# Performance work log

Measured on AMD Instinct MI355X. Metric: run time of the kernel, lower is better.

Reference implementation:

```python
import jax, jax.numpy as jnp
import numpy as np
from jax import lax

NUM_LAYERS = 3
NUM_QUBITS = 8
BATCH = 131072
DIM = 2 ** NUM_QUBITS  # 256


def _rot_mats(params):
    # params: (L, Q, 3) angles for RX, RY, RZ. Returns combined U = RZ @ RY @ RX, (L, Q, 2, 2) complex64.
    half = params * 0.5
    cx = jnp.cos(half[..., 0]).astype(jnp.complex64)
    sx = jnp.sin(half[..., 0]).astype(jnp.complex64)
    cy = jnp.cos(half[..., 1]).astype(jnp.complex64)
    sy = jnp.sin(half[..., 1]).astype(jnp.complex64)
    ezm = jnp.exp(-1j * half[..., 2]).astype(jnp.complex64)
    ezp = jnp.exp(1j * half[..., 2]).astype(jnp.complex64)
    zero = jnp.zeros_like(cx)
    RX = jnp.stack([jnp.stack([cx, -1j * sx], -1), jnp.stack([-1j * sx, cx], -1)], -2)
    RY = jnp.stack([jnp.stack([cy, -sy], -1), jnp.stack([sy, cy], -1)], -2)
    RZ = jnp.stack([jnp.stack([ezm, zero], -1), jnp.stack([zero, ezp], -1)], -2)
    return jnp.einsum('lqij,lqjk,lqkm->lqim', RZ, RY, RX)


def _apply_1q(state, U, wire):
    # state: (B, 2,2,...,2); wire w lives on axis w+1 (PennyLane wire 0 = most significant bit)
    ax = wire + 1
    return jnp.moveaxis(jnp.tensordot(U, state, axes=((1,), (ax,))), 0, ax)


def _apply_cnot(state, ctrl, tgt):
    c_ax, t_ax = ctrl + 1, tgt + 1
    s0 = lax.index_in_dim(state, 0, axis=c_ax, keepdims=True)
    s1 = lax.index_in_dim(state, 1, axis=c_ax, keepdims=True)
    s1 = jnp.flip(s1, axis=t_ax)
    return jnp.concatenate([s0, s1], axis=c_ax)


def _circuit(params, state_re, state_im):
    U = _rot_mats(params)  # (L, Q, 2, 2)
    state = (state_re + 1j * state_im).astype(jnp.complex64)
    state = state.reshape((state.shape[0],) + (2,) * NUM_QUBITS)
    for l in range(NUM_LAYERS):
        for q in range(NUM_QUBITS):
            state = _apply_1q(state, U[l, q], q)
        for q in range(NUM_QUBITS):
            state = _apply_cnot(state, q, (q + 1) % NUM_QUBITS)
    state = state.reshape(state.shape[0], DIM)
    # probability that wire 0 measures |0>: sum |amp|^2 over first half of amplitudes
    half = state[:, : DIM // 2]
    return jnp.sum(half.real ** 2 + half.imag ** 2, axis=1).astype(jnp.float32)


def setup_inputs() -> dict:
    key = jax.random.key(0)
    k1, k2, k3 = jax.random.split(key, 3)
    params = jax.random.uniform(k1, (NUM_LAYERS, NUM_QUBITS, 3), dtype=jnp.float32)
    sr = jax.random.normal(k2, (BATCH, DIM), dtype=jnp.float32)
    si = jax.random.normal(k3, (BATCH, DIM), dtype=jnp.float32)
    norm = jnp.sqrt(jnp.sum(sr ** 2 + si ** 2, axis=1, keepdims=True))
    return {"params": params, "state_re": sr / norm, "state_im": si / norm}


def reference(params, state_re, state_im):
    return _circuit(params, state_re, state_im)
```

## Files before the change

kernel.cpp:

```cpp
#include <hip/hip_runtime.h>
#include <stdint.h>

#define NLAYERS 3
#define NQ 8
#define DIM 256
#define HALF 128
#define BATCH 131072

typedef float  f32x4  __attribute__((ext_vector_type(4)));
typedef __bf16 bf16x8 __attribute__((ext_vector_type(8)));

__device__ __forceinline__ unsigned short f2bf(float f){
    union { float f; uint32_t u; } v; v.f = f;
    uint32_t u = v.u;
    u += 0x7fffu + ((u >> 16) & 1u);
    return (unsigned short)(u >> 16);
}

__device__ __forceinline__ float2 cmul(float2 a, float2 b){
    return make_float2(a.x*b.x - a.y*b.y, a.x*b.y + a.y*b.x);
}

__device__ __forceinline__ void gload_lds16(void* lds, const void* g){
    __builtin_amdgcn_global_load_lds(
        (const __attribute__((address_space(1))) unsigned int*)g,
        (__attribute__((address_space(3))) unsigned int*)lds,
        16, 0, 0);
}

__global__ __launch_bounds__(256) void build_w_kernel(const float* __restrict__ params,
                                                      unsigned short* __restrict__ W){
    __shared__ float2 st[2][DIM];
    __shared__ float2 gm[NLAYERS*NQ][4];
    const int j = blockIdx.x;
    const int i = threadIdx.x;

    if (i < NLAYERS*NQ){
        const float* pp = params + i*3;
        float hx = 0.5f*pp[0], hy = 0.5f*pp[1], hz = 0.5f*pp[2];
        float cx = cosf(hx), sx = sinf(hx);
        float cy = cosf(hy), sy = sinf(hy);
        float cz = cosf(hz), sz = sinf(hz);
        float2 ezm = make_float2(cz, -sz), ezp = make_float2(cz, sz);
        float2 m00 = make_float2( cy*cx,  sy*sx);
        float2 m01 = make_float2(-sy*cx, -cy*sx);
        float2 m10 = make_float2( sy*cx, -cy*sx);
        float2 m11 = make_float2( cy*cx, -sy*sx);
        gm[i][0] = cmul(ezm, m00);
        gm[i][1] = cmul(ezm, m01);
        gm[i][2] = cmul(ezp, m10);
        gm[i][3] = cmul(ezp, m11);
    }

    int psrc = i;
    #pragma unroll
    for (int q = NQ-1; q >= 0; --q){
        int c  = 7 - q;
        int tb = 7 - ((q + 1) & 7);
        psrc = ((psrc >> c) & 1) ? (psrc ^ (1 << tb)) : psrc;
    }

    int cur = 0;
    st[0][i] = make_float2(i == j ? 1.0f : 0.0f, 0.0f);
    __syncthreads();

    for (int l = 0; l < NLAYERS; ++l){
        for (int q = 0; q < NQ; ++q){
            float2 U0a = gm[l*NQ+q][0], U0b = gm[l*NQ+q][1];
            float2 U1a = gm[l*NQ+q][2], U1b = gm[l*NQ+q][3];
            int p  = 7 - q;
            int bs = (i >> p) & 1;
            int i0 = i & ~(1 << p), i1 = i | (1 << p);
            float2 a0 = st[cur][i0], a1 = st[cur][i1];
            float2 ua = bs ? U1a : U0a;
            float2 ub = bs ? U1b : U0b;
            float2 r;
            r.x = ua.x*a0.x - ua.y*a0.y + ub.x*a1.x - ub.y*a1.y;
            r.y = ua.x*a0.y + ua.y*a0.x + ub.x*a1.y + ub.y*a1.x;
            st[cur ^ 1][i] = r;
            cur ^= 1;
            __syncthreads();
        }
        float2 r = st[cur][psrc];
        st[cur ^ 1][i] = r;
        cur ^= 1;
        __syncthreads();
    }

    const int m = i & 127;
    float2 a = st[cur][m];
    const uint32_t off = (uint32_t)m*256u
                       + ((((uint32_t)j >> 3) ^ ((uint32_t)m & 7u)) << 3)
                       + ((uint32_t)j & 7u);
    if (i < 128) W[off]          = f2bf(a.x);
    else         W[32768u + off] = f2bf(a.y);
}

__global__ __launch_bounds__(1024) void qform2_kernel(const float* __restrict__ sr,
                                                      const float* __restrict__ si,
                                                      const unsigned short* __restrict__ W,
                                                      float* __restrict__ out){
    __shared__ unsigned short Bs[65536];

    const int tid  = threadIdx.x;
    const int lane = tid & 63;
    const int w    = tid >> 6;
    const int l15  = lane & 15;
    const int quad = lane >> 4;

    #pragma unroll
    for (int r = 0; r < 8; ++r){
        const int c = w*8 + r;
        gload_lds16(&Bs[c*512], W + (size_t)c*512 + lane*8);
    }
    __syncthreads();

    const size_t row0 = (size_t)blockIdx.x * 512 + (size_t)w * 32;

    #pragma unroll 1
    for (int t = 0; t < 2; ++t){
        const float* ar = sr + (row0 + (size_t)(t*16 + l15)) * DIM;
        const float* ai = si + (row0 + (size_t)(t*16 + l15)) * DIM;

        f32x4 accR[8], accI[8];
        const f32x4 z = {0.0f, 0.0f, 0.0f, 0.0f};
        #pragma unroll
        for (int jf = 0; jf < 8; ++jf){ accR[jf] = z; accI[jf] = z; }

        float4 r0 = *(const float4*)(ar + quad*8);
        float4 r1 = *(const float4*)(ar + quad*8 + 4);
        float4 q0 = *(const float4*)(ai + quad*8);
        float4 q1 = *(const float4*)(ai + quad*8 + 4);

        #pragma unroll 1
        for (int ks = 0; ks < 8; ++ks){
            union { float4 v; uint32_t u[4]; } ha, hb;
            union { uint32_t u[4]; bf16x8 f; } pr, pi, pn;
            ha.v = r0; hb.v = r1;
            pr.u[0] = __builtin_amdgcn_perm(ha.u[1], ha.u[0], 0x07060302);
            pr.u[1] = __builtin_amdgcn_perm(ha.u[3], ha.u[2], 0x07060302);
            pr.u[2] = __builtin_amdgcn_perm(hb.u[1], hb.u[0], 0x07060302);
            pr.u[3] = __builtin_amdgcn_perm(hb.u[3], hb.u[2], 0x07060302);
            ha.v = q0; hb.v = q1;
            pi.u[0] = __builtin_amdgcn_perm(ha.u[1], ha.u[0], 0x07060302);
            pi.u[1] = __builtin_amdgcn_perm(ha.u[3], ha.u[2], 0x07060302);
            pi.u[2] = __builtin_amdgcn_perm(hb.u[1], hb.u[0], 0x07060302);
            pi.u[3] = __builtin_amdgcn_perm(hb.u[3], hb.u[2], 0x07060302);
            pn.u[0] = pi.u[0] ^ 0x80008000u;
            pn.u[1] = pi.u[1] ^ 0x80008000u;
            pn.u[2] = pi.u[2] ^ 0x80008000u;
            pn.u[3] = pi.u[3] ^ 0x80008000u;
            const bf16x8 fr = pr.f;
            const bf16x8 fi = pi.f;
            const bf16x8 fn = pn.f;

            const int nk = (ks < 7) ? (ks + 1) : 7;
            r0 = *(const float4*)(ar + nk*32 + quad*8);
            r1 = *(const float4*)(ar + nk*32 + quad*8 + 4);
            q0 = *(const float4*)(ai + nk*32 + quad*8);
            q1 = *(const float4*)(ai + nk*32 + quad*8 + 4);

            const int ub = l15*256 + (((ks*4 + quad) ^ (l15 & 7)) << 3);

            #pragma unroll
            for (int jf = 0; jf < 8; ++jf){
                const bf16x8 br = *(const bf16x8*)&Bs[ub + jf*4096];
                const bf16x8 bi = *(const bf16x8*)&Bs[32768 + ub + jf*4096];
                accR[jf] = __builtin_amdgcn_mfma_f32_16x16x32_bf16(fr, br, accR[jf], 0, 0, 0);
                accR[jf] = __builtin_amdgcn_mfma_f32_16x16x32_bf16(fn, bi, accR[jf], 0, 0, 0);
                accI[jf] = __builtin_amdgcn_mfma_f32_16x16x32_bf16(fr, bi, accI[jf], 0, 0, 0);
                accI[jf] = __builtin_amdgcn_mfma_f32_16x16x32_bf16(fi, br, accI[jf], 0, 0, 0);
            }
        }

        float s[4];
        #pragma unroll
        for (int r = 0; r < 4; ++r){
            float tt = 0.0f;
            #pragma unroll
            for (int jf = 0; jf < 8; ++jf){
                const float vr = accR[jf][r];
                const float vi = accI[jf][r];
                tt += vr*vr + vi*vi;
            }
            tt += __shfl_xor(tt, 1);
            tt += __shfl_xor(tt, 2);
            tt += __shfl_xor(tt, 4);
            tt += __shfl_xor(tt, 8);
            s[r] = tt;
        }
        if (l15 == 0){
            float4 o; o.x = s[0]; o.y = s[1]; o.z = s[2]; o.w = s[3];
            *(float4*)(out + row0 + t*16 + quad*4) = o;
        }
    }
}

extern "C" void kernel_launch(void* const* d_in, const int* in_sizes, int n_in,
                              void* d_out, int out_size, void* d_ws, size_t ws_size,
                              hipStream_t stream){
    const float* params = (const float*)d_in[0];
    const float* sr     = (const float*)d_in[1];
    const float* si     = (const float*)d_in[2];
    unsigned short* Wimg = (unsigned short*)d_ws;
    float* out          = (float*)d_out;

    build_w_kernel<<<dim3(DIM), dim3(256), 0, stream>>>(params, Wimg);
    qform2_kernel<<<dim3(256), dim3(1024), 0, stream>>>(sr, si, Wimg, out);
}
```

Measured before the change: 297.5 us.

## Deepen global prefetch to four stages across fully unrolled K loop

Merges the two row-tile iterations into one fully unrolled loop of 16 K-steps. It keeps four stages of register prefetch in flight, so global loads for step k+4 are issued while step k computes, and loads for the second tile start before the first tile's reduction. It also raises wave priority around the MFMA block with s_setprio. The cost is higher register pressure from 16 extra float4 buffers plus the full unroll, which may reduce occupancy or cause spills.

```diff
diff --git a/kernel.cpp b/kernel.cpp
--- a/kernel.cpp
+++ b/kernel.cpp
@@ -107,6 +107,7 @@
     const int w    = tid >> 6;
     const int l15  = lane & 15;
     const int quad = lane >> 4;
+    const int xq   = l15 & 7;
 
     #pragma unroll
     for (int r = 0; r < 8; ++r){
@@ -116,82 +117,101 @@
     __syncthreads();
 
     const size_t row0 = (size_t)blockIdx.x * 512 + (size_t)w * 32;
-
-    #pragma unroll 1
-    for (int t = 0; t < 2; ++t){
-        const float* ar = sr + (row0 + (size_t)(t*16 + l15)) * DIM;
-        const float* ai = si + (row0 + (size_t)(t*16 + l15)) * DIM;
-
-        f32x4 accR[8], accI[8];
-        const f32x4 z = {0.0f, 0.0f, 0.0f, 0.0f};
+    const float* ar0 = sr + (row0 + l15) * DIM;
+    const float* ai0 = si + (row0 + l15) * DIM;
+    const float* ar1 = ar0 + (size_t)16 * DIM;
+    const float* ai1 = ai0 + (size_t)16 * DIM;
+
+    f32x4 accR[8], accI[8];
+    const f32x4 z = {0.0f, 0.0f, 0.0f, 0.0f};
+    #pragma unroll
+    for (int jf = 0; jf < 8; ++jf){ accR[jf] = z; accI[jf] = z; }
+
+    float4 R0[4], R1[4], Q0[4], Q1[4];
+
+    #pragma unroll
+    for (int p = 0; p < 4; ++p){
+        R0[p] = *(const float4*)(ar0 + p*32 + quad*8);
+        R1[p] = *(const float4*)(ar0 + p*32 + quad*8 + 4);
+        Q0[p] = *(const float4*)(ai0 + p*32 + quad*8);
+        Q1[p] = *(const float4*)(ai0 + p*32 + quad*8 + 4);
+    }
+
+    #pragma unroll
+    for (int kab = 0; kab < 16; ++kab){
+        const int ks = kab & 7;
+        const int s  = kab & 3;
+
+        union { float4 v; uint32_t u[4]; } ha, hb;
+        union { uint32_t u[4]; bf16x8 f; } pr, pi, pn;
+        ha.v = R0[s]; hb.v = R1[s];
+        pr.u[0] = __builtin_amdgcn_perm(ha.u[1], ha.u[0], 0x07060302);
+        pr.u[1] = __builtin_amdgcn_perm(ha.u[3], ha.u[2], 0x07060302);
+        pr.u[2] = __builtin_amdgcn_perm(hb.u[1], hb.u[0], 0x07060302);
+        pr.u[3] = __builtin_amdgcn_perm(hb.u[3], hb.u[2], 0x07060302);
+        ha.v = Q0[s]; hb.v = Q1[s];
+        pi.u[0] = __builtin_amdgcn_perm(ha.u[1], ha.u[0], 0x07060302);
+        pi.u[1] = __builtin_amdgcn_perm(ha.u[3], ha.u[2], 0x07060302);
+        pi.u[2] = __builtin_amdgcn_perm(hb.u[1], hb.u[0], 0x07060302);
+        pi.u[3] = __builtin_amdgcn_perm(hb.u[3], hb.u[2], 0x07060302);
+        pn.u[0] = pi.u[0] ^ 0x80008000u;
+        pn.u[1] = pi.u[1] ^ 0x80008000u;
+        pn.u[2] = pi.u[2] ^ 0x80008000u;
+        pn.u[3] = pi.u[3] ^ 0x80008000u;
+        const bf16x8 fr = pr.f;
+        const bf16x8 fi = pi.f;
+        const bf16x8 fn = pn.f;
+
+        if (kab + 4 < 16){
+            const int nk = kab + 4;
+            const float* pra = (nk < 8) ? ar0 : ar1;
+            const float* pia = (nk < 8) ? ai0 : ai1;
+            const int kk = nk & 7;
+            R0[s] = *(const float4*)(pra + kk*32 + quad*8);
+            R1[s] = *(const float4*)(pra + kk*32 + quad*8 + 4);
+            Q0[s] = *(const float4*)(pia + kk*32 + quad*8);
+            Q1[s] = *(const float4*)(pia + kk*32 + quad*8 + 4);
+        }
+
+        const int ub = l15*256 + ((((ks<<2) + quad) ^ xq) << 3);
+        __builtin_amdgcn_s_setprio(1);
         #pragma unroll
-        for (int jf = 0; jf < 8; ++jf){ accR[jf] = z; accI[jf] = z; }
-
-        float4 r0 = *(const float4*)(ar + quad*8);
-        float4 r1 = *(const float4*)(ar + quad*8 + 4);
-        float4 q0 = *(const float4*)(ai + quad*8);
-        float4 q1 = *(const float4*)(ai + quad*8 + 4);
-
-        #pragma unroll 1
-        for (int ks = 0; ks < 8; ++ks){
-            union { float4 v; uint32_t u[4]; } ha, hb;
-            union { uint32_t u[4]; bf16x8 f; } pr, pi, pn;
-            ha.v = r0; hb.v = r1;
-            pr.u[0] = __builtin_amdgcn_perm(ha.u[1], ha.u[0], 0x07060302);
-            pr.u[1] = __builtin_amdgcn_perm(ha.u[3], ha.u[2], 0x07060302);
-            pr.u[2] = __builtin_amdgcn_perm(hb.u[1], hb.u[0], 0x07060302);
-            pr.u[3] = __builtin_amdgcn_perm(hb.u[3], hb.u[2], 0x07060302);
-            ha.v = q0; hb.v = q1;
-            pi.u[0] = __builtin_amdgcn_perm(ha.u[1], ha.u[0], 0x07060302);
-            pi.u[1] = __builtin_amdgcn_perm(ha.u[3], ha.u[2], 0x07060302);
-            pi.u[2] = __builtin_amdgcn_perm(hb.u[1], hb.u[0], 0x07060302);
-            pi.u[3] = __builtin_amdgcn_perm(hb.u[3], hb.u[2], 0x07060302);
-            pn.u[0] = pi.u[0] ^ 0x80008000u;
-            pn.u[1] = pi.u[1] ^ 0x80008000u;
-            pn.u[2] = pi.u[2] ^ 0x80008000u;
-            pn.u[3] = pi.u[3] ^ 0x80008000u;
-            const bf16x8 fr = pr.f;
-            const bf16x8 fi = pi.f;
-            const bf16x8 fn = pn.f;
-
-            const int nk = (ks < 7) ? (ks + 1) : 7;
-            r0 = *(const float4*)(ar + nk*32 + quad*8);
-            r1 = *(const float4*)(ar + nk*32 + quad*8 + 4);
-            q0 = *(const float4*)(ai + nk*32 + quad*8);
-            q1 = *(const float4*)(ai + nk*32 + quad*8 + 4);
-
-            const int ub = l15*256 + (((ks*4 + quad) ^ (l15 & 7)) << 3);
-
+        for (int jf = 0; jf < 8; ++jf){
+            const bf16x8 br = *(const bf16x8*)&Bs[ub + jf*4096];
+            const bf16x8 bi = *(const bf16x8*)&Bs[32768 + ub + jf*4096];
+            accR[jf] = __builtin_amdgcn_mfma_f32_16x16x32_bf16(fr, br, accR[jf], 0, 0, 0);
+            accR[jf] = __builtin_amdgcn_mfma_f32_16x16x32_bf16(fn, bi, accR[jf], 0, 0, 0);
+            accI[jf] = __builtin_amdgcn_mfma_f32_16x16x32_bf16(fr, bi, accI[jf], 0, 0, 0);
+            accI[jf] = __builtin_amdgcn_mfma_f32_16x16x32_bf16(fi, br, accI[jf], 0, 0, 0);
+        }
+        __builtin_amdgcn_s_setprio(0);
+
+        if (ks == 7){
+            const int t = kab >> 3;
+            float sacc[4];
             #pragma unroll
-            for (int jf = 0; jf < 8; ++jf){
-                const bf16x8 br = *(const bf16x8*)&Bs[ub + jf*4096];
-                const bf16x8 bi = *(const bf16x8*)&Bs[32768 + ub + jf*4096];
-                accR[jf] = __builtin_amdgcn_mfma_f32_16x16x32_bf16(fr, br, accR[jf], 0, 0, 0);
-                accR[jf] = __builtin_amdgcn_mfma_f32_16x16x32_bf16(fn, bi, accR[jf], 0, 0, 0);
-                accI[jf] = __builtin_amdgcn_mfma_f32_16x16x32_bf16(fr, bi, accI[jf], 0, 0, 0);
-                accI[jf] = __builtin_amdgcn_mfma_f32_16x16x32_bf16(fi, br, accI[jf], 0, 0, 0);
+            for (int r = 0; r < 4; ++r){
+                float tt = 0.0f;
+                #pragma unroll
+                for (int jf = 0; jf < 8; ++jf){
+                    const float vr = accR[jf][r];
+                    const float vi = accI[jf][r];
+                    tt += vr*vr + vi*vi;
+                }
+                tt += __shfl_xor(tt, 1);
+                tt += __shfl_xor(tt, 2);
+                tt += __shfl_xor(tt, 4);
+                tt += __shfl_xor(tt, 8);
+                sacc[r] = tt;
             }
-        }
-
-        float s[4];
-        #pragma unroll
-        for (int r = 0; r < 4; ++r){
-            float tt = 0.0f;
-            #pragma unroll
-            for (int jf = 0; jf < 8; ++jf){
-                const float vr = accR[jf][r];
-                const float vi = accI[jf][r];
-                tt += vr*vr + vi*vi;
+            if (l15 == 0){
+                float4 o; o.x = sacc[0]; o.y = sacc[1]; o.z = sacc[2]; o.w = sacc[3];
+                *(float4*)(out + row0 + t*16 + quad*4) = o;
             }
-            tt += __shfl_xor(tt, 1);
-            tt += __shfl_xor(tt, 2);
-            tt += __shfl_xor(tt, 4);
-            tt += __shfl_xor(tt, 8);
-            s[r] = tt;
-        }
-        if (l15 == 0){
-            float4 o; o.x = s[0]; o.y = s[1]; o.z = s[2]; o.w = s[3];
-            *(float4*)(out + row0 + t*16 + quad*4) = o;
+            if (t == 0){
+                #pragma unroll
+                for (int jf = 0; jf < 8; ++jf){ accR[jf] = z; accI[jf] = z; }
+            }
         }
     }
 }
```

New measurement: 336.3 us. 13.1% more time.

## Deepen row prefetch to a full 16-row tile with 512-thread blocks

Applied to the files above, without the earlier changes.

Each block drops to 512 threads (8 waves), and each wave now handles 64 rows in four 16-row tiles instead of 32 rows in two. The loads for the next tile, all eight K-slices of it, are issued in register slots as each slice is consumed, so a whole tile is in flight instead of one slice ahead. MFMA sections get raised wave priority through s_setprio. The aim is to hide HBM latency on the streaming input reads, at the cost of much higher register pressure and fewer waves per CU to hide latency with.

```diff
diff --git a/kernel.cpp b/kernel.cpp
--- a/kernel.cpp
+++ b/kernel.cpp
@@ -96,10 +96,56 @@
     else         W[32768u + off] = f2bf(a.y);
 }
 
-__global__ __launch_bounds__(1024) void qform2_kernel(const float* __restrict__ sr,
-                                                      const float* __restrict__ si,
-                                                      const unsigned short* __restrict__ W,
-                                                      float* __restrict__ out){
+
+#define LOADSLOT(S, PR, PI)                          \
+    sR0_##S = *(const float4*)((PR) + (S)*32);       \
+    sR1_##S = *(const float4*)((PR) + (S)*32 + 4);   \
+    sQ0_##S = *(const float4*)((PI) + (S)*32);       \
+    sQ1_##S = *(const float4*)((PI) + (S)*32 + 4);
+
+#define STEP(S)                                                                 \
+{                                                                               \
+    union { float4 v; uint32_t u[4]; } ha_, hb_;                                \
+    union { uint32_t u[4]; bf16x8 f; } pr_, pi_, pn_;                           \
+    ha_.v = sR0_##S; hb_.v = sR1_##S;                                           \
+    pr_.u[0] = __builtin_amdgcn_perm(ha_.u[1], ha_.u[0], 0x07060302);           \
+    pr_.u[1] = __builtin_amdgcn_perm(ha_.u[3], ha_.u[2], 0x07060302);           \
+    pr_.u[2] = __builtin_amdgcn_perm(hb_.u[1], hb_.u[0], 0x07060302);           \
+    pr_.u[3] = __builtin_amdgcn_perm(hb_.u[3], hb_.u[2], 0x07060302);           \
+    ha_.v = sQ0_##S; hb_.v = sQ1_##S;                                           \
+    pi_.u[0] = __builtin_amdgcn_perm(ha_.u[1], ha_.u[0], 0x07060302);           \
+    pi_.u[1] = __builtin_amdgcn_perm(ha_.u[3], ha_.u[2], 0x07060302);           \
+    pi_.u[2] = __builtin_amdgcn_perm(hb_.u[1], hb_.u[0], 0x07060302);           \
+    pi_.u[3] = __builtin_amdgcn_perm(hb_.u[3], hb_.u[2], 0x07060302);           \
+    pn_.u[0] = pi_.u[0] ^ 0x80008000u;                                          \
+    pn_.u[1] = pi_.u[1] ^ 0x80008000u;                                          \
+    pn_.u[2] = pi_.u[2] ^ 0x80008000u;                                          \
+    pn_.u[3] = pi_.u[3] ^ 0x80008000u;                                          \
+    const bf16x8 fr_ = pr_.f;                                     \
+    const bf16x8 fi_ = pi_.f;                                     \
+    const bf16x8 fn_ = pn_.f;                                    \
+      \
+    LOADSLOT(S, narq, naiq)                                                     \
+    const int ub_ = l15*256 + ((((S<<2) + quad) ^ xq) << 3);                    \
+    const unsigned short* bre_ = &Bs[ub_];                                      \
+    const unsigned short* bim_ = &Bs[32768 + ub_];                              \
+    __builtin_amdgcn_s_setprio(1);                                              \
+    _Pragma("unroll")                                                           \
+    for (int jf = 0; jf < 8; ++jf){                                             \
+        const bf16x8 br = *(const bf16x8*)(bre_ + jf*4096);                     \
+        const bf16x8 bi = *(const bf16x8*)(bim_ + jf*4096);                     \
+        accR[jf] = __builtin_amdgcn_mfma_f32_16x16x32_bf16(fr_, br, accR[jf], 0, 0, 0); \
+        accR[jf] = __builtin_amdgcn_mfma_f32_16x16x32_bf16(fn_, bi, accR[jf], 0, 0, 0); \
+        accI[jf] = __builtin_amdgcn_mfma_f32_16x16x32_bf16(fr_, bi, accI[jf], 0, 0, 0); \
+        accI[jf] = __builtin_amdgcn_mfma_f32_16x16x32_bf16(fi_, br, accI[jf], 0, 0, 0); \
+    }                                                                           \
+    __builtin_amdgcn_s_setprio(0);                                              \
+}
+
+__global__ __launch_bounds__(512, 2) void qform2_kernel(const float* __restrict__ sr,
+                                                        const float* __restrict__ si,
+                                                        const unsigned short* __restrict__ W,
+                                                        float* __restrict__ out){
     __shared__ unsigned short Bs[65536];
 
     const int tid  = threadIdx.x;
@@ -107,92 +153,86 @@
     const int w    = tid >> 6;
     const int l15  = lane & 15;
     const int quad = lane >> 4;
+    const int xq   = l15 & 7;
+
+    const size_t rowbase = (size_t)blockIdx.x * 512 + (size_t)w * 64;
+
+    const float* arq = sr + (rowbase + l15) * DIM + quad*8;
+    const float* aiq = si + (rowbase + l15) * DIM + quad*8;
+
+    float4 sR0_0, sR1_0, sQ0_0, sQ1_0;
+    float4 sR0_1, sR1_1, sQ0_1, sQ1_1;
+    float4 sR0_2, sR1_2, sQ0_2, sQ1_2;
+    float4 sR0_3, sR1_3, sQ0_3, sQ1_3;
+    float4 sR0_4, sR1_4, sQ0_4, sQ1_4;
+    float4 sR0_5, sR1_5, sQ0_5, sQ1_5;
+    float4 sR0_6, sR1_6, sQ0_6, sQ1_6;
+    float4 sR0_7, sR1_7, sQ0_7, sQ1_7;
+
+    LOADSLOT(0, arq, aiq)
+    LOADSLOT(1, arq, aiq)
+    LOADSLOT(2, arq, aiq)
+    LOADSLOT(3, arq, aiq)
+    LOADSLOT(4, arq, aiq)
+    LOADSLOT(5, arq, aiq)
+    LOADSLOT(6, arq, aiq)
+    LOADSLOT(7, arq, aiq)
 
     #pragma unroll
-    for (int r = 0; r < 8; ++r){
-        const int c = w*8 + r;
+    for (int r = 0; r < 16; ++r){
+        const int c = w*16 + r;
         gload_lds16(&Bs[c*512], W + (size_t)c*512 + lane*8);
     }
     __syncthreads();
 
-    const size_t row0 = (size_t)blockIdx.x * 512 + (size_t)w * 32;
+    f32x4 accR[8], accI[8];
+    const f32x4 z = {0.0f, 0.0f, 0.0f, 0.0f};
+    #pragma unroll
+    for (int jf = 0; jf < 8; ++jf){ accR[jf] = z; accI[jf] = z; }
 
     #pragma unroll 1
-    for (int t = 0; t < 2; ++t){
-        const float* ar = sr + (row0 + (size_t)(t*16 + l15)) * DIM;
-        const float* ai = si + (row0 + (size_t)(t*16 + l15)) * DIM;
-
-        f32x4 accR[8], accI[8];
-        const f32x4 z = {0.0f, 0.0f, 0.0f, 0.0f};
-        #pragma unroll
-        for (int jf = 0; jf < 8; ++jf){ accR[jf] = z; accI[jf] = z; }
-
-        float4 r0 = *(const float4*)(ar + quad*8);
-        float4 r1 = *(const float4*)(ar + quad*8 + 4);
-        float4 q0 = *(const float4*)(ai + quad*8);
-        float4 q1 = *(const float4*)(ai + quad*8 + 4);
-
-        #pragma unroll 1
-        for (int ks = 0; ks < 8; ++ks){
-            union { float4 v; uint32_t u[4]; } ha, hb;
-            union { uint32_t u[4]; bf16x8 f; } pr, pi, pn;
-            ha.v = r0; hb.v = r1;
-            pr.u[0] = __builtin_amdgcn_perm(ha.u[1], ha.u[0], 0x07060302);
-            pr.u[1] = __builtin_amdgcn_perm(ha.u[3], ha.u[2], 0x07060302);
-            pr.u[2] = __builtin_amdgcn_perm(hb.u[1], hb.u[0], 0x07060302);
-            pr.u[3] = __builtin_amdgcn_perm(hb.u[3], hb.u[2], 0x07060302);
-            ha.v = q0; hb.v = q1;
-            pi.u[0] = __builtin_amdgcn_perm(ha.u[1], ha.u[0], 0x07060302);
-            pi.u[1] = __builtin_amdgcn_perm(ha.u[3], ha.u[2], 0x07060302);
-            pi.u[2] = __builtin_amdgcn_perm(hb.u[1], hb.u[0], 0x07060302);
-            pi.u[3] = __builtin_amdgcn_perm(hb.u[3], hb.u[2], 0x07060302);
-            pn.u[0] = pi.u[0] ^ 0x80008000u;
-            pn.u[1] = pi.u[1] ^ 0x80008000u;
-            pn.u[2] = pi.u[2] ^ 0x80008000u;
-            pn.u[3] = pi.u[3] ^ 0x80008000u;
-            const bf16x8 fr = pr.f;
-            const bf16x8 fi = pi.f;
-            const bf16x8 fn = pn.f;
-
-            const int nk = (ks < 7) ? (ks + 1) : 7;
-            r0 = *(const float4*)(ar + nk*32 + quad*8);
-            r1 = *(const float4*)(ar + nk*32 + quad*8 + 4);
-            q0 = *(const float4*)(ai + nk*32 + quad*8);
-            q1 = *(const float4*)(ai + nk*32 + quad*8 + 4);
-
-            const int ub = l15*256 + (((ks*4 + quad) ^ (l15 & 7)) << 3);
-
+    for (int t = 0; t < 4; ++t){
+        const float* narq = (t < 3) ? (arq + 16*DIM) : arq;
+        const float* naiq = (t < 3) ? (aiq + 16*DIM) : aiq;
+
+        STEP(0)
+        STEP(1)
+        STEP(2)
+        STEP(3)
+        STEP(4)
+        STEP(5)
+        STEP(6)
+        STEP(7)
+
+        {
+            float sacc[4];
             #pragma unroll
-            for (int jf = 0; jf < 8; ++jf){
-                const bf16x8 br = *(const bf16x8*)&Bs[ub + jf*4096];
-                const bf16x8 bi = *(const bf16x8*)&Bs[32768 + ub + jf*4096];
-                accR[jf] = __builtin_amdgcn_mfma_f32_16x16x32_bf16(fr, br, accR[jf], 0, 0, 0);
-                accR[jf] = __builtin_amdgcn_mfma_f32_16x16x32_bf16(fn, bi, accR[jf], 0, 0, 0);
-                accI[jf] = __builtin_amdgcn_mfma_f32_16x16x32_bf16(fr, bi, accI[jf], 0, 0, 0);
-                accI[jf] = __builtin_amdgcn_mfma_f32_16x16x32_bf16(fi, br, accI[jf], 0, 0, 0);
+            for (int r = 0; r < 4; ++r){
+                float tt = 0.0f;
+                #pragma unroll
+                for (int jf = 0; jf < 8; ++jf){
+                    const float vr = accR[jf][r];
+                    const float vi = accI[jf][r];
+                    tt += vr*vr + vi*vi;
+                }
+                tt += __shfl_xor(tt, 1);
+                tt += __shfl_xor(tt, 2);
+                tt += __shfl_xor(tt, 4);
+                tt += __shfl_xor(tt, 8);
+                sacc[r] = tt;
+            }
+            if (l15 == 0){
+                float4 o; o.x = sacc[0]; o.y = sacc[1]; o.z = sacc[2]; o.w = sacc[3];
+                *(float4*)(out + rowbase + t*16 + quad*4) = o;
+            }
+            if (t < 3){
+                #pragma unroll
+                for (int jf = 0; jf < 8; ++jf){ accR[jf] = z; accI[jf] = z; }
             }
         }
 
-        float s[4];
-        #pragma unroll
-        for (int r = 0; r < 4; ++r){
-            float tt = 0.0f;
-            #pragma unroll
-            for (int jf = 0; jf < 8; ++jf){
-                const float vr = accR[jf][r];
-                const float vi = accI[jf][r];
-                tt += vr*vr + vi*vi;
-            }
-            tt += __shfl_xor(tt, 1);
-            tt += __shfl_xor(tt, 2);
-            tt += __shfl_xor(tt, 4);
-            tt += __shfl_xor(tt, 8);
-            s[r] = tt;
-        }
-        if (l15 == 0){
-            float4 o; o.x = s[0]; o.y = s[1]; o.z = s[2]; o.w = s[3];
-            *(float4*)(out + row0 + t*16 + quad*4) = o;
-        }
+        arq = narq;
+        aiq = naiq;
     }
 }
 
@@ -206,5 +246,5 @@
     float* out          = (float*)d_out;
 
     build_w_kernel<<<dim3(DIM), dim3(256), 0, stream>>>(params, Wimg);
-    qform2_kernel<<<dim3(256), dim3(1024), 0, stream>>>(sr, si, Wimg, out);
-}
+    qform2_kernel<<<dim3(256), dim3(512), 0, stream>>>(sr, si, Wimg, out);
+}
```

After: 471.4 us. 58.5% more time.

## Keep W fragments in registers and stream A tiles via double-buffered LDS

Applied to the files above, without the earlier changes.

Reorganizes the GEMM so each wave holds a fixed 16-column slice of the W matrix in registers, while input rows are staged into double-buffered LDS through global_load_lds. Per-row partial sums are reduced across waves through shared memory. The W layout loses its swizzle, and the launch goes from 256 blocks of 1024 threads to 512 blocks of 512 threads. The aim is to remove heavy LDS reads of W and the scattered global loads of A, and to overlap loading with MFMA work. In exchange it adds two barriers per tile and a cross-wave reduction.

```diff
diff --git a/kernel.cpp b/kernel.cpp
--- a/kernel.cpp
+++ b/kernel.cpp
@@ -4,7 +4,6 @@
 #define NLAYERS 3
 #define NQ 8
 #define DIM 256
-#define HALF 128
 #define BATCH 131072
 
 typedef float  f32x4  __attribute__((ext_vector_type(4)));
@@ -89,110 +88,131 @@
 
     const int m = i & 127;
     float2 a = st[cur][m];
-    const uint32_t off = (uint32_t)m*256u
-                       + ((((uint32_t)j >> 3) ^ ((uint32_t)m & 7u)) << 3)
-                       + ((uint32_t)j & 7u);
-    if (i < 128) W[off]          = f2bf(a.x);
-    else         W[32768u + off] = f2bf(a.y);
-}
-
-__global__ __launch_bounds__(1024) void qform2_kernel(const float* __restrict__ sr,
-                                                      const float* __restrict__ si,
-                                                      const unsigned short* __restrict__ W,
-                                                      float* __restrict__ out){
-    __shared__ unsigned short Bs[65536];
+    if (i < 128) W[(uint32_t)m*256u + (uint32_t)j]          = f2bf(a.x);
+    else         W[32768u + (uint32_t)m*256u + (uint32_t)j] = f2bf(a.y);
+}
+
+
+#define STAGE(B) { \
+    gload_lds16(&Abuf[B][(r0+0)*DIM], srcp0); srcp0 += 16*DIM; \
+    gload_lds16(&Abuf[B][(r0+1)*DIM], srcp1); srcp1 += 16*DIM; \
+    gload_lds16(&Abuf[B][(r0+2)*DIM], srcp2); srcp2 += 16*DIM; \
+    gload_lds16(&Abuf[B][(r0+3)*DIM], srcp3); srcp3 += 16*DIM; }
+
+#define BSTEP(S) { \
+    f32x4 ra0 = *(const f32x4*)(arow + S*32 + o0); \
+    f32x4 ra1 = *(const f32x4*)(arow + S*32 + o1); \
+    f32x4 qa0 = *(const f32x4*)(irow + S*32 + o0); \
+    f32x4 qa1 = *(const f32x4*)(irow + S*32 + o1); \
+    union { f32x4 v; uint32_t u[4]; } ha_, hb_; \
+    union { uint32_t u[4]; bf16x8 f; } pr_, pi_, pn_; \
+    ha_.v = ra0; hb_.v = ra1; \
+    pr_.u[0] = __builtin_amdgcn_perm(ha_.u[1], ha_.u[0], 0x07060302); \
+    pr_.u[1] = __builtin_amdgcn_perm(ha_.u[3], ha_.u[2], 0x07060302); \
+    pr_.u[2] = __builtin_amdgcn_perm(hb_.u[1], hb_.u[0], 0x07060302); \
+    pr_.u[3] = __builtin_amdgcn_perm(hb_.u[3], hb_.u[2], 0x07060302); \
+    ha_.v = qa0; hb_.v = qa1; \
+    pi_.u[0] = __builtin_amdgcn_perm(ha_.u[1], ha_.u[0], 0x07060302); \
+    pi_.u[1] = __builtin_amdgcn_perm(ha_.u[3], ha_.u[2], 0x07060302); \
+    pi_.u[2] = __builtin_amdgcn_perm(hb_.u[1], hb_.u[0], 0x07060302); \
+    pi_.u[3] = __builtin_amdgcn_perm(hb_.u[3], hb_.u[2], 0x07060302); \
+    pn_.u[0] = pi_.u[0] ^ 0x80008000u; \
+    pn_.u[1] = pi_.u[1] ^ 0x80008000u; \
+    pn_.u[2] = pi_.u[2] ^ 0x80008000u; \
+    pn_.u[3] = pi_.u[3] ^ 0x80008000u; \
+    accR = __builtin_amdgcn_mfma_f32_16x16x32_bf16(pr_.f, bre_##S, accR, 0, 0, 0); \
+    accR = __builtin_amdgcn_mfma_f32_16x16x32_bf16(pn_.f, bim_##S, accR, 0, 0, 0); \
+    accI = __builtin_amdgcn_mfma_f32_16x16x32_bf16(pr_.f, bim_##S, accI, 0, 0, 0); \
+    accI = __builtin_amdgcn_mfma_f32_16x16x32_bf16(pi_.f, bre_##S, accI, 0, 0, 0); \
+}
+
+__global__ __launch_bounds__(512, 4) void qform3_kernel(const float* __restrict__ sr,
+                                                        const float* __restrict__ si,
+                                                        const unsigned short* __restrict__ W,
+                                                        float* __restrict__ out){
+    __shared__ float Abuf[2][32*DIM];
+    __shared__ float red[128];
 
     const int tid  = threadIdx.x;
     const int lane = tid & 63;
     const int w    = tid >> 6;
     const int l15  = lane & 15;
     const int quad = lane >> 4;
-
-    #pragma unroll
-    for (int r = 0; r < 8; ++r){
-        const int c = w*8 + r;
-        gload_lds16(&Bs[c*512], W + (size_t)c*512 + lane*8);
-    }
-    __syncthreads();
-
-    const size_t row0 = (size_t)blockIdx.x * 512 + (size_t)w * 32;
-
+    const int x7   = l15 & 7;
+    const size_t m0 = (size_t)blockIdx.x * 256;
+
+    const int r0 = w * 4;
+    const float* plane = (w < 4) ? sr : si;
+    const float* srcp0 = plane + (m0 + ((r0+0)&15))*DIM + ((lane ^ ((r0+0)&7)) << 2);
+    const float* srcp1 = plane + (m0 + ((r0+1)&15))*DIM + ((lane ^ ((r0+1)&7)) << 2);
+    const float* srcp2 = plane + (m0 + ((r0+2)&15))*DIM + ((lane ^ ((r0+2)&7)) << 2);
+    const float* srcp3 = plane + (m0 + ((r0+3)&15))*DIM + ((lane ^ ((r0+3)&7)) << 2);
+
+    STAGE(0)
+
+    const unsigned short* wre = W + ((uint32_t)(w*16 + l15))*256u + (uint32_t)(quad*8);
+    const unsigned short* wim = wre + 32768u;
+    const bf16x8 bre_0 = *(const bf16x8*)(wre + 0*32);
+    const bf16x8 bre_1 = *(const bf16x8*)(wre + 1*32);
+    const bf16x8 bre_2 = *(const bf16x8*)(wre + 2*32);
+    const bf16x8 bre_3 = *(const bf16x8*)(wre + 3*32);
+    const bf16x8 bre_4 = *(const bf16x8*)(wre + 4*32);
+    const bf16x8 bre_5 = *(const bf16x8*)(wre + 5*32);
+    const bf16x8 bre_6 = *(const bf16x8*)(wre + 6*32);
+    const bf16x8 bre_7 = *(const bf16x8*)(wre + 7*32);
+    const bf16x8 bim_0 = *(const bf16x8*)(wim + 0*32);
+    const bf16x8 bim_1 = *(const bf16x8*)(wim + 1*32);
+    const bf16x8 bim_2 = *(const bf16x8*)(wim + 2*32);
+    const bf16x8 bim_3 = *(const bf16x8*)(wim + 3*32);
+    const bf16x8 bim_4 = *(const bf16x8*)(wim + 4*32);
+    const bf16x8 bim_5 = *(const bf16x8*)(wim + 5*32);
+    const bf16x8 bim_6 = *(const bf16x8*)(wim + 6*32);
+    const bf16x8 bim_7 = *(const bf16x8*)(wim + 7*32);
+
+    const int o0 = (((quad << 1)    ) ^ x7) << 2;
+    const int o1 = (((quad << 1) | 1) ^ x7) << 2;
+
+    int buf = 0;
     #pragma unroll 1
-    for (int t = 0; t < 2; ++t){
-        const float* ar = sr + (row0 + (size_t)(t*16 + l15)) * DIM;
-        const float* ai = si + (row0 + (size_t)(t*16 + l15)) * DIM;
-
-        f32x4 accR[8], accI[8];
-        const f32x4 z = {0.0f, 0.0f, 0.0f, 0.0f};
-        #pragma unroll
-        for (int jf = 0; jf < 8; ++jf){ accR[jf] = z; accI[jf] = z; }
-
-        float4 r0 = *(const float4*)(ar + quad*8);
-        float4 r1 = *(const float4*)(ar + quad*8 + 4);
-        float4 q0 = *(const float4*)(ai + quad*8);
-        float4 q1 = *(const float4*)(ai + quad*8 + 4);
-
-        #pragma unroll 1
-        for (int ks = 0; ks < 8; ++ks){
-            union { float4 v; uint32_t u[4]; } ha, hb;
-            union { uint32_t u[4]; bf16x8 f; } pr, pi, pn;
-            ha.v = r0; hb.v = r1;
-            pr.u[0] = __builtin_amdgcn_perm(ha.u[1], ha.u[0], 0x07060302);
-            pr.u[1] = __builtin_amdgcn_perm(ha.u[3], ha.u[2], 0x07060302);
-            pr.u[2] = __builtin_amdgcn_perm(hb.u[1], hb.u[0], 0x07060302);
-            pr.u[3] = __builtin_amdgcn_perm(hb.u[3], hb.u[2], 0x07060302);
-            ha.v = q0; hb.v = q1;
-            pi.u[0] = __builtin_amdgcn_perm(ha.u[1], ha.u[0], 0x07060302);
-            pi.u[1] = __builtin_amdgcn_perm(ha.u[3], ha.u[2], 0x07060302);
-            pi.u[2] = __builtin_amdgcn_perm(hb.u[1], hb.u[0], 0x07060302);
-            pi.u[3] = __builtin_amdgcn_perm(hb.u[3], hb.u[2], 0x07060302);
-            pn.u[0] = pi.u[0] ^ 0x80008000u;
-            pn.u[1] = pi.u[1] ^ 0x80008000u;
-            pn.u[2] = pi.u[2] ^ 0x80008000u;
-            pn.u[3] = pi.u[3] ^ 0x80008000u;
-            const bf16x8 fr = pr.f;
-            const bf16x8 fi = pi.f;
-            const bf16x8 fn = pn.f;
-
-            const int nk = (ks < 7) ? (ks + 1) : 7;
-            r0 = *(const float4*)(ar + nk*32 + quad*8);
-            r1 = *(const float4*)(ar + nk*32 + quad*8 + 4);
-            q0 = *(const float4*)(ai + nk*32 + quad*8);
-            q1 = *(const float4*)(ai + nk*32 + quad*8 + 4);
-
-            const int ub = l15*256 + (((ks*4 + quad) ^ (l15 & 7)) << 3);
-
-            #pragma unroll
-            for (int jf = 0; jf < 8; ++jf){
-                const bf16x8 br = *(const bf16x8*)&Bs[ub + jf*4096];
-                const bf16x8 bi = *(const bf16x8*)&Bs[32768 + ub + jf*4096];
-                accR[jf] = __builtin_amdgcn_mfma_f32_16x16x32_bf16(fr, br, accR[jf], 0, 0, 0);
-                accR[jf] = __builtin_amdgcn_mfma_f32_16x16x32_bf16(fn, bi, accR[jf], 0, 0, 0);
-                accI[jf] = __builtin_amdgcn_mfma_f32_16x16x32_bf16(fr, bi, accI[jf], 0, 0, 0);
-                accI[jf] = __builtin_amdgcn_mfma_f32_16x16x32_bf16(fi, br, accI[jf], 0, 0, 0);
-            }
-        }
-
-        float s[4];
+    for (int t = 0; t < 16; ++t){
+        if (t < 15){
+            STAGE(buf ^ 1)
+            asm volatile("s_waitcnt vmcnt(4)" ::: "memory");
+        } else {
+            asm volatile("s_waitcnt vmcnt(0)" ::: "memory");
+        }
+        __builtin_amdgcn_s_barrier();
+        __builtin_amdgcn_sched_barrier(0);
+
+        const float* arow = &Abuf[buf][l15 * DIM];
+        const float* irow = &Abuf[buf][(16 + l15) * DIM];
+
+        f32x4 accR = {0.0f, 0.0f, 0.0f, 0.0f};
+        f32x4 accI = {0.0f, 0.0f, 0.0f, 0.0f};
+        BSTEP(0) BSTEP(1) BSTEP(2) BSTEP(3)
+        BSTEP(4) BSTEP(5) BSTEP(6) BSTEP(7)
+
         #pragma unroll
         for (int r = 0; r < 4; ++r){
-            float tt = 0.0f;
-            #pragma unroll
-            for (int jf = 0; jf < 8; ++jf){
-                const float vr = accR[jf][r];
-                const float vi = accI[jf][r];
-                tt += vr*vr + vi*vi;
-            }
+            const float vr = accR[r], vi = accI[r];
+            float tt = vr*vr + vi*vi;
             tt += __shfl_xor(tt, 1);
             tt += __shfl_xor(tt, 2);
             tt += __shfl_xor(tt, 4);
             tt += __shfl_xor(tt, 8);
-            s[r] = tt;
-        }
-        if (l15 == 0){
-            float4 o; o.x = s[0]; o.y = s[1]; o.z = s[2]; o.w = s[3];
-            *(float4*)(out + row0 + t*16 + quad*4) = o;
-        }
+            if (l15 == 0) red[w*16 + quad*4 + r] = tt;
+        }
+        asm volatile("s_waitcnt lgkmcnt(0)" ::: "memory");
+        __builtin_amdgcn_s_barrier();
+        __builtin_amdgcn_sched_barrier(0);
+
+        if (tid < 16){
+            float o = 0.0f;
+            #pragma unroll
+            for (int ww = 0; ww < 8; ++ww) o += red[ww*16 + tid];
+            out[m0 + t*16 + tid] = o;
+        }
+        buf ^= 1;
     }
 }
 
@@ -206,5 +226,5 @@
     float* out          = (float*)d_out;
 
     build_w_kernel<<<dim3(DIM), dim3(256), 0, stream>>>(params, Wimg);
-    qform2_kernel<<<dim3(256), dim3(1024), 0, stream>>>(sr, si, Wimg, out);
-}
+    qform3_kernel<<<dim3(512), dim3(512), 0, stream>>>(sr, si, Wimg, out);
+}
```

New measurement: 294.7 us. About the same (-0.9%).
